# Kernel optimization log

Hardware: AMD Instinct MI355X
Metric: run time of the kernel (lower is better)

The kernel has to match this reference:

```python
import jax, jax.numpy as jnp
import numpy as np

MAX_BLUR = 20.0
MIN_BLUR = 0.5
MIN_SCALE = 0.001


def _dct_matrix(N, dtype):
    """Orthonormal DCT-II matrix C: dct(v) = C @ v (matches torch_dct norm='ortho')."""
    n = jnp.arange(N, dtype=dtype)
    k = n[:, None]
    C = jnp.cos(jnp.pi * (n[None, :] + 0.5) * k / N)
    scale = jnp.where(k == 0, jnp.sqrt(jnp.asarray(1.0 / N, dtype)), jnp.sqrt(jnp.asarray(2.0 / N, dtype)))
    return C * scale


def setup_inputs() -> dict:
    key = jax.random.key(0)
    k1, k2 = jax.random.split(key)
    x = jax.random.normal(k1, (128, 3, 256, 256), dtype=jnp.float32)
    t = jax.random.uniform(k2, (128,), dtype=jnp.float32)
    return {"x": x, "t": t}


def reference(x, t):
    dtype = x.dtype
    N = x.shape[-1]
    # frequency grid: pi * linspace(0, N-1, N) / N, squared and summed over 2D
    freqs = jnp.pi * jnp.arange(N, dtype=dtype) / N
    freq_sq = freqs[:, None] ** 2 + freqs[None, :] ** 2  # [N, N]

    # blur schedule: exp(log(min_blur)*(1-t) + log(max_blur)*t)
    sigmas = jnp.exp(np.log(MIN_BLUR) * (1.0 - t) + np.log(MAX_BLUR) * t)
    sigmas = sigmas[:, None, None, None]  # [B,1,1,1]
    tau = sigmas ** 2 / 2

    fade_freq = jnp.exp(-freq_sq * tau)  # [B,1,N,N]
    fade_freq = jnp.where(fade_freq < 0.01, jnp.zeros((), dtype), fade_freq)

    C = _dct_matrix(N, dtype)  # [N, N]
    # separable 2D DCT-II (ortho): out[k,n] = sum_{h,w} C[k,h] C[n,w] x[h,w]
    dct_x = jnp.einsum('kh,nw,bchw->bckn', C, C, x)
    blurred_dct = dct_x * (fade_freq * (1.0 - MIN_SCALE) + MIN_SCALE)
    # inverse 2D DCT (ortho): transpose matrices
    blurred_x = jnp.einsum('kh,nw,bckn->bchw', C, C, blurred_dct)
    return blurred_x.astype(dtype)
```

## Files before the change

### kernel.cpp

```cpp
#include <hip/hip_runtime.h>
#include <hip/hip_fp16.h>

typedef _Float16 f16;
typedef _Float16 f16x8 __attribute__((ext_vector_type(8)));
typedef _Float16 f16x4 __attribute__((ext_vector_type(4)));
typedef float f32x4 __attribute__((ext_vector_type(4)));

#define NSZ 256
#define NIMG 384

__device__ __forceinline__ int sw(int r, int c) {
  return r * NSZ + (c ^ ((r & 7) << 3));
}

__global__ void prep_kernel(f16* __restrict__ Cm, f16* __restrict__ CTm,
                            float* __restrict__ g, const float* __restrict__ t) {
  int k = blockIdx.x;
  int h = threadIdx.x;
  double scale = (k == 0) ? 0.0625 : 0.08838834764831844;
  double val = cos(3.14159265358979323846 * ((double)h + 0.5) * (double)k / 256.0) * scale;
  f16 vh = (f16)((float)val);
  Cm[k * NSZ + h] = vh;
  CTm[h * NSZ + k] = vh;
  if (k < 128) {
    float tb = t[k];
    float sg = expf(-0.69314718055994531f * (1.0f - tb) + 2.99573227355399099f * tb);
    float tau = 0.5f * sg * sg;
    float f = 3.14159265358979f * (float)h / 256.0f;
    g[k * NSZ + h] = expf(-f * f * tau);
  }
}

template <bool OP1_LDS>
__device__ __forceinline__ void do_gemm(const f16* L, const f16* __restrict__ T,
                                        int r0, int c0, int lrow, int lk,
                                        f32x4 (&acc)[8][4]) {
#pragma unroll
  for (int fi = 0; fi < 8; ++fi)
#pragma unroll
    for (int fj = 0; fj < 4; ++fj) {
      f32x4 z = {0.f, 0.f, 0.f, 0.f};
      acc[fi][fj] = z;
    }
  for (int ks = 0; ks < 8; ++ks) {
    int kh = ks * 32 + lk;
    f16x8 o1[8], o2[4];
#pragma unroll
    for (int fi = 0; fi < 8; ++fi) {
      int row = r0 + fi * 16 + lrow;
      if constexpr (OP1_LDS)
        o1[fi] = *(const f16x8*)&L[sw(row, kh)];
      else
        o1[fi] = *(const f16x8*)&T[row * NSZ + kh];
    }
#pragma unroll
    for (int fj = 0; fj < 4; ++fj) {
      int row = c0 + fj * 16 + lrow;
      if constexpr (OP1_LDS)
        o2[fj] = *(const f16x8*)&T[row * NSZ + kh];
      else
        o2[fj] = *(const f16x8*)&L[sw(row, kh)];
    }
#pragma unroll
    for (int fi = 0; fi < 8; ++fi)
#pragma unroll
      for (int fj = 0; fj < 4; ++fj)
        acc[fi][fj] = __builtin_amdgcn_mfma_f32_16x16x32_f16(o1[fi], o2[fj], acc[fi][fj], 0, 0, 0);
  }
}

__device__ __forceinline__ void writeT(f16* L, int r0, int c0, int lrow, int lv4,
                                       const f32x4 (&acc)[8][4]) {
#pragma unroll
  for (int fi = 0; fi < 8; ++fi) {
    int rp = r0 + fi * 16 + lv4;
#pragma unroll
    for (int fj = 0; fj < 4; ++fj) {
      int c = c0 + fj * 16 + lrow;
      f16x4 h;
      h[0] = (f16)acc[fi][fj][0];
      h[1] = (f16)acc[fi][fj][1];
      h[2] = (f16)acc[fi][fj][2];
      h[3] = (f16)acc[fi][fj][3];
      *(f16x4*)&L[sw(c, rp)] = h;
    }
  }
}

__global__ __launch_bounds__(512, 1) void fused_kernel(
    const float* __restrict__ x, float* __restrict__ out,
    const f16* __restrict__ Cm, const f16* __restrict__ CTm,
    const float* __restrict__ g) {
  __shared__ f16 L[NSZ * NSZ];

  const int img = blockIdx.x;
  const int b = img / 3;
  const float* X = x + (size_t)img * NSZ * NSZ;
  float* Y = out + (size_t)img * NSZ * NSZ;

  const int t = threadIdx.x;
  const int lane = t & 63;
  const int wave = t >> 6;
  const int wr = wave >> 2;
  const int wc = wave & 3;
  const int r0 = wr * 128;
  const int c0 = wc * 64;
  const int lrow = lane & 15;
  const int lk = (lane >> 4) * 8;
  const int lv4 = (lane >> 4) * 4;

  for (int it = 0; it < 16; ++it) {
    int gid = it * 512 + t;
    int r = gid >> 5;
    int c8 = (gid & 31) << 3;
    const float* s = X + r * NSZ + c8;
    float4 a0 = *(const float4*)s;
    float4 a1 = *(const float4*)(s + 4);
    f16x8 v;
    v[0] = (f16)a0.x; v[1] = (f16)a0.y; v[2] = (f16)a0.z; v[3] = (f16)a0.w;
    v[4] = (f16)a1.x; v[5] = (f16)a1.y; v[6] = (f16)a1.z; v[7] = (f16)a1.w;
    *(f16x8*)&L[sw(r, c8)] = v;
  }
  __syncthreads();

  f32x4 acc[8][4];

  do_gemm<true>(L, Cm, r0, c0, lrow, lk, acc);
  __syncthreads();
  writeT(L, r0, c0, lrow, lv4, acc);
  __syncthreads();

  do_gemm<false>(L, Cm, r0, c0, lrow, lk, acc);
  {
    const float* gb = g + b * NSZ;
#pragma unroll
    for (int fi = 0; fi < 8; ++fi) {
      float4 gk = *(const float4*)&gb[r0 + fi * 16 + lv4];
      float gkv[4] = {gk.x, gk.y, gk.z, gk.w};
#pragma unroll
      for (int fj = 0; fj < 4; ++fj) {
        float gn = gb[c0 + fj * 16 + lrow];
#pragma unroll
        for (int v = 0; v < 4; ++v) {
          float fade = gkv[v] * gn;
          float s = (fade < 0.01f) ? 0.001f : (fade * 0.999f + 0.001f);
          acc[fi][fj][v] *= s;
        }
      }
    }
  }
  __syncthreads();
  writeT(L, r0, c0, lrow, lv4, acc);
  __syncthreads();

  do_gemm<true>(L, CTm, r0, c0, lrow, lk, acc);
  __syncthreads();
  writeT(L, r0, c0, lrow, lv4, acc);
  __syncthreads();

  do_gemm<true>(L, CTm, r0, c0, lrow, lk, acc);
#pragma unroll
  for (int fi = 0; fi < 8; ++fi) {
    int r = r0 + fi * 16 + lv4;
#pragma unroll
    for (int fj = 0; fj < 4; ++fj) {
      int c = c0 + fj * 16 + lrow;
#pragma unroll
      for (int v = 0; v < 4; ++v)
        Y[(size_t)(r + v) * NSZ + c] = acc[fi][fj][v];
    }
  }
}

extern "C" void kernel_launch(void* const* d_in, const int* in_sizes, int n_in,
                              void* d_out, int out_size, void* d_ws, size_t ws_size,
                              hipStream_t stream) {
  const float* x = (const float*)d_in[0];
  const float* t = (const float*)d_in[1];
  float* out = (float*)d_out;

  char* ws = (char*)d_ws;
  float* g = (float*)ws;
  f16* Cm = (f16*)(ws + 131072);
  f16* CTm = (f16*)(ws + 262144);

  prep_kernel<<<256, 256, 0, stream>>>(Cm, CTm, g, t);
  fused_kernel<<<NIMG, 512, 0, stream>>>(x, out, Cm, CTm, g);
}
```

Measured before the change: 121.1 us.

## Split DCT blur into two kernels, truncate to nonzero frequency band, add MIN_SCALE identity

```diff
diff --git a/kernel.cpp b/kernel.cpp
--- a/kernel.cpp
+++ b/kernel.cpp
@@ -14,7 +14,8 @@
 }
 
 __global__ void prep_kernel(f16* __restrict__ Cm, f16* __restrict__ CTm,
-                            float* __restrict__ g, const float* __restrict__ t) {
+                            float* __restrict__ g, int* __restrict__ Kq,
+                            const float* __restrict__ t) {
   int k = blockIdx.x;
   int h = threadIdx.x;
   double scale = (k == 0) ? 0.0625 : 0.08838834764831844;
@@ -22,153 +23,230 @@
   f16 vh = (f16)((float)val);
   Cm[k * NSZ + h] = vh;
   CTm[h * NSZ + k] = vh;
+  int pred = 0;
   if (k < 128) {
     float tb = t[k];
     float sg = expf(-0.69314718055994531f * (1.0f - tb) + 2.99573227355399099f * tb);
     float tau = 0.5f * sg * sg;
     float f = 3.14159265358979f * (float)h / 256.0f;
-    g[k * NSZ + h] = expf(-f * f * tau);
-  }
-}
-
-template <bool OP1_LDS>
-__device__ __forceinline__ void do_gemm(const f16* L, const f16* __restrict__ T,
-                                        int r0, int c0, int lrow, int lk,
-                                        f32x4 (&acc)[8][4]) {
-#pragma unroll
-  for (int fi = 0; fi < 8; ++fi)
-#pragma unroll
-    for (int fj = 0; fj < 4; ++fj) {
-      f32x4 z = {0.f, 0.f, 0.f, 0.f};
-      acc[fi][fj] = z;
-    }
-  for (int ks = 0; ks < 8; ++ks) {
+    float gv = expf(-f * f * tau);
+    g[k * NSZ + h] = gv;
+    pred = (gv >= 0.0099f) ? 1 : 0;
+  }
+  int cnt = __syncthreads_count(pred);
+  if (k < 128 && h == 0) {
+    int K = ((cnt + 63) >> 6) << 6;
+    if (K < 64) K = 64;
+    if (K > 256) K = 256;
+    Kq[k] = K;
+  }
+}
+
+__global__ __launch_bounds__(512, 4) void kernelA(
+    const float* __restrict__ x, f16* __restrict__ Ep,
+    const f16* __restrict__ Cm, const float* __restrict__ g,
+    const int* __restrict__ Kq_arr) {
+  __shared__ char smem[69632];
+  f16* P1 = (f16*)smem;
+  f16* Xs = (f16*)(smem + 32768);
+
+  int bid0 = blockIdx.x;
+  int bid = (bid0 & 7) * 192 + (bid0 >> 3);
+  int img = bid >> 2, nb = bid & 3;
+  int b = img / 3;
+  int Kq = Kq_arr[b];
+  if (nb * 64 >= Kq) return;
+
+  int t = threadIdx.x, lane = t & 63, wave = t >> 6;
+  int lrow = lane & 15, lk = (lane >> 4) * 8, lv4 = (lane >> 4) * 4;
+  const float* X = x + (size_t)img * 65536;
+
+  int hi = wave >> 1, ni = wave & 1;
+  for (int hc = 0; hc < 4; ++hc) {
+    if (hc) __syncthreads();
+#pragma unroll
+    for (int c = 0; c < 4; ++c) {
+      int gid = t + c * 512;
+      int r = gid >> 5, c8 = (gid & 31) << 3;
+      const float* s = X + (hc * 64 + r) * NSZ + c8;
+      float4 a0 = *(const float4*)s;
+      float4 a1 = *(const float4*)(s + 4);
+      f16x8 v;
+      v[0] = (f16)a0.x; v[1] = (f16)a0.y; v[2] = (f16)a0.z; v[3] = (f16)a0.w;
+      v[4] = (f16)a1.x; v[5] = (f16)a1.y; v[6] = (f16)a1.z; v[7] = (f16)a1.w;
+      *(f16x8*)&Xs[sw(r, c8)] = v;
+    }
+    __syncthreads();
+    f32x4 accP[2];
+#pragma unroll
+    for (int j = 0; j < 2; ++j) { f32x4 z = {0.f, 0.f, 0.f, 0.f}; accP[j] = z; }
+    for (int ks = 0; ks < 8; ++ks) {
+      int kh = ks * 32 + lk;
+      f16x8 o1 = *(const f16x8*)&Xs[sw(hi * 16 + lrow, kh)];
+#pragma unroll
+      for (int j = 0; j < 2; ++j) {
+        int n = nb * 64 + ni * 32 + j * 16 + lrow;
+        f16x8 o2 = *(const f16x8*)&Cm[n * NSZ + kh];
+        accP[j] = __builtin_amdgcn_mfma_f32_16x16x32_f16(o1, o2, accP[j], 0, 0, 0);
+      }
+    }
+#pragma unroll
+    for (int j = 0; j < 2; ++j) {
+      int n_loc = ni * 32 + j * 16 + lrow;
+      int hp = hc * 64 + hi * 16 + lv4;
+      f16x4 hv;
+      hv[0] = (f16)accP[j][0]; hv[1] = (f16)accP[j][1];
+      hv[2] = (f16)accP[j][2]; hv[3] = (f16)accP[j][3];
+      *(f16x4*)&P1[sw(n_loc, hp)] = hv;
+    }
+  }
+  __syncthreads();
+
+  f16* Est = (f16*)Xs;
+  int kb0 = wave * 32;
+  if (kb0 < Kq) {
+    f32x4 accE[2][4];
+#pragma unroll
+    for (int i = 0; i < 2; ++i)
+#pragma unroll
+      for (int j = 0; j < 4; ++j) { f32x4 z = {0.f, 0.f, 0.f, 0.f}; accE[i][j] = z; }
+    for (int ks = 0; ks < 8; ++ks) {
+      int kh = ks * 32 + lk;
+      f16x8 o1[2], o2[4];
+#pragma unroll
+      for (int i = 0; i < 2; ++i)
+        o1[i] = *(const f16x8*)&Cm[(kb0 + i * 16 + lrow) * NSZ + kh];
+#pragma unroll
+      for (int j = 0; j < 4; ++j)
+        o2[j] = *(const f16x8*)&P1[sw(j * 16 + lrow, kh)];
+#pragma unroll
+      for (int i = 0; i < 2; ++i)
+#pragma unroll
+        for (int j = 0; j < 4; ++j)
+          accE[i][j] = __builtin_amdgcn_mfma_f32_16x16x32_f16(o1[i], o2[j], accE[i][j], 0, 0, 0);
+    }
+    const float* gb = g + b * NSZ;
+#pragma unroll
+    for (int i = 0; i < 2; ++i) {
+#pragma unroll
+      for (int j = 0; j < 4; ++j) {
+        float gn = gb[nb * 64 + j * 16 + lrow];
+#pragma unroll
+        for (int v = 0; v < 4; ++v) {
+          int k = kb0 + i * 16 + lv4 + v;
+          float fade = gb[k] * gn;
+          float s = (fade < 0.01f) ? 0.f : 0.999f * fade;
+          Est[k * 72 + j * 16 + lrow] = (f16)(accE[i][j][v] * s);
+        }
+      }
+    }
+  }
+  __syncthreads();
+  f16* Eout = Ep + (size_t)img * 65536 + nb * 64;
+  for (int gg = t; gg < Kq * 8; gg += 512) {
+    int k = gg >> 3, gn = gg & 7;
+    f16x8 v = *(const f16x8*)&Est[k * 72 + gn * 8];
+    *(f16x8*)&Eout[k * NSZ + gn * 8] = v;
+  }
+}
+
+__global__ __launch_bounds__(512, 4) void kernelB(
+    const float* __restrict__ x, const f16* __restrict__ Ep,
+    float* __restrict__ out, const f16* __restrict__ CTm,
+    const int* __restrict__ Kq_arr) {
+  __shared__ char smem[69632];
+  f16* Ech = (f16*)smem;
+  f16* Qt = (f16*)(smem + 32768);
+  float* Yt = (float*)smem;
+
+  int bid0 = blockIdx.x;
+  int bid = (bid0 & 7) * 192 + (bid0 >> 3);
+  int img = bid >> 2, wb = bid & 3;
+  int b = img / 3;
+  int Kq = Kq_arr[b];
+  int nks = Kq >> 5, nkc = Kq >> 6;
+
+  int t = threadIdx.x, lane = t & 63, wave = t >> 6;
+  int lrow = lane & 15, lk = (lane >> 4) * 8, lv4 = (lane >> 4) * 4;
+  const float* X = x + (size_t)img * 65536;
+
+  int ki = wave >> 1, wj = wave & 1;
+  for (int kc = 0; kc < nkc; ++kc) {
+    __syncthreads();
+    {
+      int k = t >> 3, sub = t & 7;
+      int gpr = Kq >> 3;
+      const f16* src = Ep + (size_t)img * 65536 + (kc * 64 + k) * NSZ;
+      for (int gg = sub; gg < gpr; gg += 8) {
+        f16x8 v = *(const f16x8*)&src[gg * 8];
+        *(f16x8*)&Ech[sw(k, gg * 8)] = v;
+      }
+    }
+    __syncthreads();
+    f32x4 accQ[2];
+#pragma unroll
+    for (int j = 0; j < 2; ++j) { f32x4 z = {0.f, 0.f, 0.f, 0.f}; accQ[j] = z; }
+    for (int ks = 0; ks < nks; ++ks) {
+      int kh = ks * 32 + lk;
+      f16x8 o1 = *(const f16x8*)&Ech[sw(ki * 16 + lrow, kh)];
+#pragma unroll
+      for (int j = 0; j < 2; ++j) {
+        int w = wb * 64 + wj * 32 + j * 16 + lrow;
+        f16x8 o2 = *(const f16x8*)&CTm[w * NSZ + kh];
+        accQ[j] = __builtin_amdgcn_mfma_f32_16x16x32_f16(o1, o2, accQ[j], 0, 0, 0);
+      }
+    }
+#pragma unroll
+    for (int j = 0; j < 2; ++j) {
+      int w_loc = wj * 32 + j * 16 + lrow;
+      int kp = kc * 64 + ki * 16 + lv4;
+      f16x4 hv;
+      hv[0] = (f16)accQ[j][0]; hv[1] = (f16)accQ[j][1];
+      hv[2] = (f16)accQ[j][2]; hv[3] = (f16)accQ[j][3];
+      *(f16x4*)&Qt[sw(w_loc, kp)] = hv;
+    }
+  }
+  __syncthreads();
+
+  f32x4 accY[2][4];
+#pragma unroll
+  for (int i = 0; i < 2; ++i)
+#pragma unroll
+    for (int j = 0; j < 4; ++j) { f32x4 z = {0.f, 0.f, 0.f, 0.f}; accY[i][j] = z; }
+  for (int ks = 0; ks < nks; ++ks) {
     int kh = ks * 32 + lk;
-    f16x8 o1[8], o2[4];
-#pragma unroll
-    for (int fi = 0; fi < 8; ++fi) {
-      int row = r0 + fi * 16 + lrow;
-      if constexpr (OP1_LDS)
-        o1[fi] = *(const f16x8*)&L[sw(row, kh)];
-      else
-        o1[fi] = *(const f16x8*)&T[row * NSZ + kh];
-    }
-#pragma unroll
-    for (int fj = 0; fj < 4; ++fj) {
-      int row = c0 + fj * 16 + lrow;
-      if constexpr (OP1_LDS)
-        o2[fj] = *(const f16x8*)&T[row * NSZ + kh];
-      else
-        o2[fj] = *(const f16x8*)&L[sw(row, kh)];
-    }
-#pragma unroll
-    for (int fi = 0; fi < 8; ++fi)
-#pragma unroll
-      for (int fj = 0; fj < 4; ++fj)
-        acc[fi][fj] = __builtin_amdgcn_mfma_f32_16x16x32_f16(o1[fi], o2[fj], acc[fi][fj], 0, 0, 0);
-  }
-}
-
-__device__ __forceinline__ void writeT(f16* L, int r0, int c0, int lrow, int lv4,
-                                       const f32x4 (&acc)[8][4]) {
-#pragma unroll
-  for (int fi = 0; fi < 8; ++fi) {
-    int rp = r0 + fi * 16 + lv4;
-#pragma unroll
-    for (int fj = 0; fj < 4; ++fj) {
-      int c = c0 + fj * 16 + lrow;
-      f16x4 h;
-      h[0] = (f16)acc[fi][fj][0];
-      h[1] = (f16)acc[fi][fj][1];
-      h[2] = (f16)acc[fi][fj][2];
-      h[3] = (f16)acc[fi][fj][3];
-      *(f16x4*)&L[sw(c, rp)] = h;
-    }
-  }
-}
-
-__global__ __launch_bounds__(512, 1) void fused_kernel(
-    const float* __restrict__ x, float* __restrict__ out,
-    const f16* __restrict__ Cm, const f16* __restrict__ CTm,
-    const float* __restrict__ g) {
-  __shared__ f16 L[NSZ * NSZ];
-
-  const int img = blockIdx.x;
-  const int b = img / 3;
-  const float* X = x + (size_t)img * NSZ * NSZ;
-  float* Y = out + (size_t)img * NSZ * NSZ;
-
-  const int t = threadIdx.x;
-  const int lane = t & 63;
-  const int wave = t >> 6;
-  const int wr = wave >> 2;
-  const int wc = wave & 3;
-  const int r0 = wr * 128;
-  const int c0 = wc * 64;
-  const int lrow = lane & 15;
-  const int lk = (lane >> 4) * 8;
-  const int lv4 = (lane >> 4) * 4;
-
-  for (int it = 0; it < 16; ++it) {
-    int gid = it * 512 + t;
-    int r = gid >> 5;
-    int c8 = (gid & 31) << 3;
-    const float* s = X + r * NSZ + c8;
-    float4 a0 = *(const float4*)s;
-    float4 a1 = *(const float4*)(s + 4);
-    f16x8 v;
-    v[0] = (f16)a0.x; v[1] = (f16)a0.y; v[2] = (f16)a0.z; v[3] = (f16)a0.w;
-    v[4] = (f16)a1.x; v[5] = (f16)a1.y; v[6] = (f16)a1.z; v[7] = (f16)a1.w;
-    *(f16x8*)&L[sw(r, c8)] = v;
-  }
-  __syncthreads();
-
-  f32x4 acc[8][4];
-
-  do_gemm<true>(L, Cm, r0, c0, lrow, lk, acc);
-  __syncthreads();
-  writeT(L, r0, c0, lrow, lv4, acc);
-  __syncthreads();
-
-  do_gemm<false>(L, Cm, r0, c0, lrow, lk, acc);
-  {
-    const float* gb = g + b * NSZ;
-#pragma unroll
-    for (int fi = 0; fi < 8; ++fi) {
-      float4 gk = *(const float4*)&gb[r0 + fi * 16 + lv4];
-      float gkv[4] = {gk.x, gk.y, gk.z, gk.w};
-#pragma unroll
-      for (int fj = 0; fj < 4; ++fj) {
-        float gn = gb[c0 + fj * 16 + lrow];
-#pragma unroll
-        for (int v = 0; v < 4; ++v) {
-          float fade = gkv[v] * gn;
-          float s = (fade < 0.01f) ? 0.001f : (fade * 0.999f + 0.001f);
-          acc[fi][fj][v] *= s;
-        }
-      }
-    }
-  }
-  __syncthreads();
-  writeT(L, r0, c0, lrow, lv4, acc);
-  __syncthreads();
-
-  do_gemm<true>(L, CTm, r0, c0, lrow, lk, acc);
-  __syncthreads();
-  writeT(L, r0, c0, lrow, lv4, acc);
-  __syncthreads();
-
-  do_gemm<true>(L, CTm, r0, c0, lrow, lk, acc);
-#pragma unroll
-  for (int fi = 0; fi < 8; ++fi) {
-    int r = r0 + fi * 16 + lv4;
-#pragma unroll
-    for (int fj = 0; fj < 4; ++fj) {
-      int c = c0 + fj * 16 + lrow;
+    f16x8 o1[2], o2[4];
+#pragma unroll
+    for (int i = 0; i < 2; ++i)
+      o1[i] = *(const f16x8*)&CTm[(wave * 32 + i * 16 + lrow) * NSZ + kh];
+#pragma unroll
+    for (int j = 0; j < 4; ++j)
+      o2[j] = *(const f16x8*)&Qt[sw(j * 16 + lrow, kh)];
+#pragma unroll
+    for (int i = 0; i < 2; ++i)
+#pragma unroll
+      for (int j = 0; j < 4; ++j)
+        accY[i][j] = __builtin_amdgcn_mfma_f32_16x16x32_f16(o1[i], o2[j], accY[i][j], 0, 0, 0);
+  }
+  __syncthreads();
+#pragma unroll
+  for (int i = 0; i < 2; ++i)
+#pragma unroll
+    for (int j = 0; j < 4; ++j)
 #pragma unroll
       for (int v = 0; v < 4; ++v)
-        Y[(size_t)(r + v) * NSZ + c] = acc[fi][fj][v];
-    }
+        Yt[(wave * 32 + i * 16 + lv4 + v) * 68 + j * 16 + lrow] = accY[i][j][v];
+  __syncthreads();
+  float* Yo = out + (size_t)img * 65536 + wb * 64;
+#pragma unroll
+  for (int it = 0; it < 8; ++it) {
+    int idx = it * 512 + t;
+    int row = idx >> 4, q = (idx & 15) * 4;
+    float4 yv = *(const float4*)&Yt[row * 68 + q];
+    float4 xv = *(const float4*)&X[row * NSZ + wb * 64 + q];
+    yv.x += 0.001f * xv.x; yv.y += 0.001f * xv.y;
+    yv.z += 0.001f * xv.z; yv.w += 0.001f * xv.w;
+    *(float4*)&Yo[row * NSZ + q] = yv;
   }
 }
 
@@ -183,7 +261,10 @@
   float* g = (float*)ws;
   f16* Cm = (f16*)(ws + 131072);
   f16* CTm = (f16*)(ws + 262144);
-
-  prep_kernel<<<256, 256, 0, stream>>>(Cm, CTm, g, t);
-  fused_kernel<<<NIMG, 512, 0, stream>>>(x, out, Cm, CTm, g);
-}
+  int* Kq = (int*)(ws + 393216);
+  f16* Ep = (f16*)(ws + 393728);
+
+  prep_kernel<<<256, 256, 0, stream>>>(Cm, CTm, g, Kq, t);
+  kernelA<<<NIMG * 4, 512, 0, stream>>>(x, Ep, Cm, g, Kq);
+  kernelB<<<NIMG * 4, 512, 0, stream>>>(x, Ep, out, CTm, Kq);
+}
```

Measured after the change: 238.5 us. +97.0%, slower.
